# Kernel tuning notes

Hardware: AMD Instinct MI355X
Metric: run time of the kernel (lower is better)

The kernel has to match this reference:

```python
import jax, jax.numpy as jnp
import numpy as np

N_NODES = 50000


def _gcn_conv(h, src, dst, W, b):
    # h: [N, d_in] -> [N, d_out]; symmetric-normalized aggregation with self-loops
    N = h.shape[0]
    h = h @ W  # transform first (d_out < d_in), like PyG GCNConv
    deg = jax.ops.segment_sum(jnp.ones_like(dst, dtype=h.dtype), dst, num_segments=N)
    dinv = jnp.where(deg > 0, jax.lax.rsqrt(jnp.maximum(deg, 1.0)), 0.0)
    norm = dinv[src] * dinv[dst]  # [E']
    msg = h[src] * norm[:, None]  # [E', d_out]
    out = jax.ops.segment_sum(msg, dst, num_segments=N)
    return out + b


def setup_inputs() -> dict:
    key = jax.random.key(0)
    k1, k2, k3, k4 = jax.random.split(key, 4)
    dim_in, dim_h, dim_out, E = 512, 96, 40, 800000
    x = jax.random.normal(k1, (N_NODES, dim_in), dtype=jnp.float32)
    edge_index = jax.random.randint(k2, (2, E), 0, N_NODES, dtype=jnp.int64)
    W1 = jax.random.normal(k3, (dim_in, dim_h), dtype=jnp.float32) / np.sqrt(dim_in)
    b1 = jnp.zeros((dim_h,), dtype=jnp.float32)
    W2 = jax.random.normal(k4, (dim_h, dim_out), dtype=jnp.float32) / np.sqrt(dim_h)
    b2 = jnp.zeros((dim_out,), dtype=jnp.float32)
    return {"x": x, "edge_index": edge_index, "W1": W1, "b1": b1, "W2": W2, "b2": b2}


def reference(x, edge_index, W1, b1, W2, b2):
    N = x.shape[0]
    loops = jnp.arange(N, dtype=edge_index.dtype)
    src = jnp.concatenate([edge_index[0], loops])
    dst = jnp.concatenate([edge_index[1], loops])
    h = jax.nn.relu(_gcn_conv(x, src, dst, W1, b1))
    # dropout p=0.5 is identity in eval mode (training=False)
    logits = _gcn_conv(h, src, dst, W2, b2)
    return (logits, jax.nn.log_softmax(logits, axis=1))
```

## Files before the change

kernel.cpp:

```cpp
#include <hip/hip_runtime.h>
#include <cstdint>
#include <cstddef>

#define DIN 512
#define DH  96
#define DOUT 40

typedef __attribute__((ext_vector_type(8))) short s8v;
typedef __attribute__((ext_vector_type(4))) float f4v;

__device__ __forceinline__ ushort f2bf(float f) {
    uint u = __float_as_uint(f);
    u += 0x7fffu + ((u >> 16) & 1u);
    return (ushort)(u >> 16);
}
__device__ __forceinline__ float bflo(uint u) { return __uint_as_float(u << 16); }
__device__ __forceinline__ float bfhi(uint u) { return __uint_as_float(u & 0xffff0000u); }

__global__ __launch_bounds__(256) void k_prep(
    const float* __restrict__ W1, const float* __restrict__ W2,
    int* __restrict__ cnt, ushort* __restrict__ W1T, ushort* __restrict__ W2T, int N)
{
    int i = blockIdx.x * 256 + threadIdx.x;
    if (i < N) cnt[i] = 0;
    if (i < DIN * DH) {
        int k = i / DH, n = i % DH;
        W1T[(size_t)n * DIN + k] = f2bf(W1[i]);
    }
    if (i < 48 * DH) {
        int n = i / DH, k = i % DH;
        W2T[i] = (n < DOUT) ? f2bf(W2[(size_t)k * DOUT + n]) : (ushort)0;
    }
}

__global__ __launch_bounds__(256) void k_hist(const int* __restrict__ dst, int* __restrict__ cnt, int E) {
    int e = blockIdx.x * 256 + threadIdx.x;
    if (e < E) atomicAdd(&cnt[dst[e]], 1);
}

__global__ __launch_bounds__(256) void k_blocksum(const int* __restrict__ cnt, int* __restrict__ bsum, int N) {
    int i = blockIdx.x * 256 + threadIdx.x;
    int c = (i < N) ? cnt[i] : 0;
    #pragma unroll
    for (int off = 32; off >= 1; off >>= 1) c += __shfl_down(c, off, 64);
    __shared__ int wsum[4];
    if ((threadIdx.x & 63) == 0) wsum[threadIdx.x >> 6] = c;
    __syncthreads();
    if (threadIdx.x == 0) bsum[blockIdx.x] = wsum[0] + wsum[1] + wsum[2] + wsum[3];
}

__global__ __launch_bounds__(256) void k_scan_small(const int* __restrict__ bsum, int* __restrict__ boff, int SB) {
    __shared__ int p[256];
    int tid = threadIdx.x;
    int v = (tid < SB) ? bsum[tid] : 0;
    p[tid] = v;
    __syncthreads();
    #pragma unroll
    for (int off = 1; off < 256; off <<= 1) {
        int t = (tid >= off) ? p[tid - off] : 0;
        __syncthreads();
        p[tid] += t;
        __syncthreads();
    }
    if (tid < SB) boff[tid] = p[tid] - v;
}

__global__ __launch_bounds__(256) void k_rowptr(
    const int* __restrict__ cnt, const int* __restrict__ boff,
    int* __restrict__ row_ptr, int* __restrict__ cursor,
    float* __restrict__ dinv, int N)
{
    __shared__ int p[256];
    int tid = threadIdx.x;
    int i = blockIdx.x * 256 + tid;
    int c = (i < N) ? cnt[i] : 0;
    p[tid] = c;
    __syncthreads();
    #pragma unroll
    for (int off = 1; off < 256; off <<= 1) {
        int t = (tid >= off) ? p[tid - off] : 0;
        __syncthreads();
        p[tid] += t;
        __syncthreads();
    }
    int excl = p[tid] - c;
    if (i < N) {
        int base = boff[blockIdx.x] + excl;
        row_ptr[i] = base;
        cursor[i]  = base;
        dinv[i] = rsqrtf(1.0f + (float)c);
        if (i == N - 1) row_ptr[N] = base + c;
    }
}

__global__ __launch_bounds__(256) void k_fill(
    const int* __restrict__ src, const int* __restrict__ dst,
    int* __restrict__ cursor, int* __restrict__ adj, int E)
{
    int e = blockIdx.x * 256 + threadIdx.x;
    if (e >= E) return;
    int pos = atomicAdd(&cursor[dst[e]], 1);
    adj[pos] = src[e];
}

#define G1_ASZ 8192
#define G1_BSZ 6144
__global__ __launch_bounds__(256) void k_gemm1(
    const float* __restrict__ x, const ushort* __restrict__ W1T,
    const float* __restrict__ dinv, ushort* __restrict__ hs1, int N)
{
    __shared__ ushort lds[2 * G1_ASZ + 2 * G1_BSZ];
    const int tid = threadIdx.x;
    const int row0 = blockIdx.x * 128;
    const int lane = tid & 63;
    const int w = tid >> 6;
    const int rb = (w >> 1) * 64;
    const int cb = (w & 1) * 48;
    const int lm = lane & 15;
    const int lq = lane >> 4;

    int aof[4][2], bof[3][2];
    #pragma unroll
    for (int i = 0; i < 4; ++i)
        #pragma unroll
        for (int ks = 0; ks < 2; ++ks) {
            int r = rb + i * 16 + lm;
            int c = ks * 32 + lq * 8;
            aof[i][ks] = r * 64 + (c ^ ((r & 7) << 3));
        }
    #pragma unroll
    for (int j = 0; j < 3; ++j)
        #pragma unroll
        for (int ks = 0; ks < 2; ++ks) {
            int n = cb + j * 16 + lm;
            int c = ks * 32 + lq * 8;
            bof[j][ks] = 2 * G1_ASZ + n * 64 + (c ^ ((n & 7) << 3));
        }

    f4v acc[4][3];
    #pragma unroll
    for (int i = 0; i < 4; ++i)
        #pragma unroll
        for (int j = 0; j < 3; ++j) acc[i][j] = (f4v)0.f;

    const int sr = tid >> 1;
    const int scb = (tid & 1) * 32;

    auto stage = [&](int kt, int buf) {
        int k0 = kt * 64;
        int gr = row0 + sr;
        ushort* A = lds + buf * G1_ASZ;
        #pragma unroll
        for (int s = 0; s < 4; ++s) {
            int c = scb + s * 8;
            float4 v0 = make_float4(0.f, 0.f, 0.f, 0.f), v1 = v0;
            if (gr < N) {
                const float* p = &x[(size_t)gr * DIN + k0 + c];
                v0 = *(const float4*)p;
                v1 = *(const float4*)(p + 4);
            }
            uint4 wv;
            wv.x = (uint)f2bf(v0.x) | ((uint)f2bf(v0.y) << 16);
            wv.y = (uint)f2bf(v0.z) | ((uint)f2bf(v0.w) << 16);
            wv.z = (uint)f2bf(v1.x) | ((uint)f2bf(v1.y) << 16);
            wv.w = (uint)f2bf(v1.z) | ((uint)f2bf(v1.w) << 16);
            *(uint4*)&A[sr * 64 + (c ^ ((sr & 7) << 3))] = wv;
        }
        ushort* B = lds + 2 * G1_ASZ + buf * G1_BSZ;
        #pragma unroll
        for (int it = 0; it < 3; ++it) {
            int ss = tid + it * 256;
            int n = ss >> 3, c = (ss & 7) * 8;
            uint4 wv = *(const uint4*)&W1T[(size_t)n * DIN + k0 + c];
            *(uint4*)&B[n * 64 + (c ^ ((n & 7) << 3))] = wv;
        }
    };

    stage(0, 0);
    for (int kt = 0; kt < 8; ++kt) {
        __syncthreads();
        if (kt < 7) stage(kt + 1, (kt + 1) & 1);
        const int ab = (kt & 1) * G1_ASZ;
        const int bb = (kt & 1) * G1_BSZ;
        #pragma unroll
        for (int ks = 0; ks < 2; ++ks) {
            s8v b0 = *(s8v*)&lds[bof[0][ks] + bb];
            s8v b1 = *(s8v*)&lds[bof[1][ks] + bb];
            s8v b2 = *(s8v*)&lds[bof[2][ks] + bb];
            #pragma unroll
            for (int i = 0; i < 4; ++i) {
                s8v a = *(s8v*)&lds[aof[i][ks] + ab];
                acc[i][0] = __builtin_amdgcn_mfma_f32_16x16x32_bf16(a, b0, acc[i][0], 0, 0, 0);
                acc[i][1] = __builtin_amdgcn_mfma_f32_16x16x32_bf16(a, b1, acc[i][1], 0, 0, 0);
                acc[i][2] = __builtin_amdgcn_mfma_f32_16x16x32_bf16(a, b2, acc[i][2], 0, 0, 0);
            }
        }
    }

    #pragma unroll
    for (int i = 0; i < 4; ++i) {
        int gr0 = row0 + rb + i * 16 + lq * 4;
        #pragma unroll
        for (int q = 0; q < 4; ++q) {
            int gr = gr0 + q;
            if (gr < N) {
                float di = dinv[gr];
                #pragma unroll
                for (int j = 0; j < 3; ++j)
                    hs1[(size_t)gr * DH + cb + j * 16 + lm] = f2bf(acc[i][j][q] * di);
            }
        }
    }
}

__global__ __launch_bounds__(256) void k_agg1(
    const int* __restrict__ row_ptr, const int* __restrict__ adj,
    const float* __restrict__ dinv, const ushort* __restrict__ hs1,
    const float* __restrict__ b1, ushort* __restrict__ h1, int N)
{
    int t = blockIdx.x * 256 + threadIdx.x;
    int node = t >> 6, lane = t & 63;
    if (node >= N) return;
    int c = lane << 1;
    const bool act = (c < DH);

    float a0 = 0.f, a1 = 0.f;
    if (act) {
        uint u = *(const uint*)&hs1[(size_t)node * DH + c];
        a0 = bflo(u); a1 = bfhi(u);
    }
    int e = row_ptr[node], e1 = row_ptr[node + 1];
    for (; e + 3 < e1; e += 4) {
        int s0 = adj[e], s1 = adj[e + 1], s2 = adj[e + 2], s3 = adj[e + 3];
        if (act) {
            uint u0 = *(const uint*)&hs1[(size_t)s0 * DH + c];
            uint u1 = *(const uint*)&hs1[(size_t)s1 * DH + c];
            uint u2 = *(const uint*)&hs1[(size_t)s2 * DH + c];
            uint u3 = *(const uint*)&hs1[(size_t)s3 * DH + c];
            a0 += bflo(u0); a1 += bfhi(u0);
            a0 += bflo(u1); a1 += bfhi(u1);
            a0 += bflo(u2); a1 += bfhi(u2);
            a0 += bflo(u3); a1 += bfhi(u3);
        }
    }
    for (; e < e1; ++e) {
        int s = adj[e];
        if (act) {
            uint u = *(const uint*)&hs1[(size_t)s * DH + c];
            a0 += bflo(u); a1 += bfhi(u);
        }
    }
    if (act) {
        float di = dinv[node];
        float r0 = fmaxf(fmaf(a0, di, b1[c]), 0.f);
        float r1 = fmaxf(fmaf(a1, di, b1[c + 1]), 0.f);
        uint wv = (uint)f2bf(r0) | ((uint)f2bf(r1) << 16);
        *(uint*)&h1[(size_t)node * DH + c] = wv;
    }
}

#define G2_HS 16384
__global__ __launch_bounds__(256) void k_gemm2(
    const ushort* __restrict__ h1, const ushort* __restrict__ W2T,
    const float* __restrict__ dinv, float* __restrict__ hs2, int N)
{
    __shared__ ushort lds[G2_HS + 48 * 128];
    const int tid = threadIdx.x;
    const int row0 = blockIdx.x * 128;

    for (int f = tid; f < 576; f += 256) {
        int r = f / 12, c = (f % 12) * 8;
        uint4 v = *(const uint4*)&W2T[r * DH + c];
        *(uint4*)&lds[G2_HS + r * 128 + (c ^ ((r & 7) << 3))] = v;
    }
    {
        int r = tid >> 1, half = tid & 1;
        int gr = row0 + r;
        #pragma unroll
        for (int i = 0; i < 6; ++i) {
            int c = half * 48 + i * 8;
            uint4 v = make_uint4(0, 0, 0, 0);
            if (gr < N) v = *(const uint4*)&h1[(size_t)gr * DH + c];
            *(uint4*)&lds[r * 128 + (c ^ ((r & 7) << 3))] = v;
        }
    }
    __syncthreads();

    const int lane = tid & 63, w = tid >> 6;
    const int rb = w * 32, lm = lane & 15, lq = lane >> 4;
    f4v acc[2][3];
    #pragma unroll
    for (int i = 0; i < 2; ++i)
        #pragma unroll
        for (int j = 0; j < 3; ++j) acc[i][j] = (f4v)0.f;

    #pragma unroll
    for (int ks = 0; ks < 3; ++ks) {
        int kk = ks * 32 + lq * 8;
        s8v b[3];
        #pragma unroll
        for (int j = 0; j < 3; ++j) {
            int n = j * 16 + lm;
            b[j] = *(s8v*)&lds[G2_HS + n * 128 + (kk ^ ((n & 7) << 3))];
        }
        #pragma unroll
        for (int i = 0; i < 2; ++i) {
            int r = rb + i * 16 + lm;
            s8v a = *(s8v*)&lds[r * 128 + (kk ^ ((r & 7) << 3))];
            #pragma unroll
            for (int j = 0; j < 3; ++j)
                acc[i][j] = __builtin_amdgcn_mfma_f32_16x16x32_bf16(a, b[j], acc[i][j], 0, 0, 0);
        }
    }

    #pragma unroll
    for (int i = 0; i < 2; ++i) {
        int gr0 = row0 + rb + i * 16 + lq * 4;
        #pragma unroll
        for (int q = 0; q < 4; ++q) {
            int gr = gr0 + q;
            if (gr < N) {
                float di = dinv[gr];
                #pragma unroll
                for (int j = 0; j < 3; ++j) {
                    int col = j * 16 + lm;
                    if (col < DOUT)
                        hs2[(size_t)gr * DOUT + col] = acc[i][j][q] * di;
                }
            }
        }
    }
}

__global__ __launch_bounds__(256) void k_agg2sm(
    const int* __restrict__ row_ptr, const int* __restrict__ adj,
    const float* __restrict__ dinv, const float* __restrict__ hs2,
    const float* __restrict__ b2, float* __restrict__ out,
    float* __restrict__ lsm, int N)
{
    int t = blockIdx.x * 256 + threadIdx.x;
    int node = t >> 6, lane = t & 63;
    if (node >= N) return;
    const bool act = lane < DOUT;

    float acc = act ? hs2[(size_t)node * DOUT + lane] : 0.f;
    int e = row_ptr[node], e1 = row_ptr[node + 1];
    for (; e + 3 < e1; e += 4) {
        int s0 = adj[e], s1 = adj[e + 1], s2 = adj[e + 2], s3 = adj[e + 3];
        if (act) {
            float v0 = hs2[(size_t)s0 * DOUT + lane];
            float v1 = hs2[(size_t)s1 * DOUT + lane];
            float v2 = hs2[(size_t)s2 * DOUT + lane];
            float v3 = hs2[(size_t)s3 * DOUT + lane];
            acc += v0 + v1 + v2 + v3;
        }
    }
    for (; e < e1; ++e) {
        int s = adj[e];
        if (act) acc += hs2[(size_t)s * DOUT + lane];
    }

    float v = act ? fmaf(acc, dinv[node], b2[lane]) : -1e30f;
    float m = v;
    #pragma unroll
    for (int off = 32; off >= 1; off >>= 1) m = fmaxf(m, __shfl_xor(m, off));
    float ex = act ? __expf(v - m) : 0.f;
    float s = ex;
    #pragma unroll
    for (int off = 32; off >= 1; off >>= 1) s += __shfl_xor(s, off);
    float lse = m + __logf(s);
    if (act) {
        out[(size_t)node * DOUT + lane] = v;
        lsm[(size_t)node * DOUT + lane] = v - lse;
    }
}

extern "C" void kernel_launch(void* const* d_in, const int* in_sizes, int n_in,
                              void* d_out, int out_size, void* d_ws, size_t ws_size,
                              hipStream_t stream) {
    const float* x  = (const float*)d_in[0];
    const int*   ei = (const int*)d_in[1];
    const float* W1 = (const float*)d_in[2];
    const float* b1 = (const float*)d_in[3];
    const float* W2 = (const float*)d_in[4];
    const float* b2 = (const float*)d_in[5];

    const int N = in_sizes[0] / DIN;
    const int E = in_sizes[1] / 2;
    const int* srcp = ei;
    const int* dstp = ei + E;
    const int SB = (N + 255) / 256;

    ushort* hs1 = (ushort*)d_ws;
    ushort* h1  = hs1 + (size_t)N * DH;
    float* hs2  = (float*)(h1 + (size_t)N * DH);
    float* dinv = hs2 + (size_t)N * DOUT;
    ushort* W1T = (ushort*)(dinv + N);
    ushort* W2T = W1T + (size_t)DH * DIN;
    int* cnt     = (int*)(W2T + 48 * DH);
    int* cursor  = cnt + N;
    int* row_ptr = cursor + N;
    int* adj     = row_ptr + N + 1;
    int* bsum    = adj + E;
    int* boff    = bsum + SB;

    float* out = (float*)d_out;
    float* lsm = out + (size_t)N * DOUT;

    const int gE = (E + 255) / 256;

    k_prep<<<SB, 256, 0, stream>>>(W1, W2, cnt, W1T, W2T, N);
    k_hist<<<gE, 256, 0, stream>>>(dstp, cnt, E);
    k_blocksum<<<SB, 256, 0, stream>>>(cnt, bsum, N);
    k_scan_small<<<1, 256, 0, stream>>>(bsum, boff, SB);
    k_rowptr<<<SB, 256, 0, stream>>>(cnt, boff, row_ptr, cursor, dinv, N);
    k_fill<<<gE, 256, 0, stream>>>(srcp, dstp, cursor, adj, E);

    k_gemm1<<<(N + 127) / 128, 256, 0, stream>>>(x, W1T, dinv, hs1, N);
    k_agg1<<<(int)(((size_t)N * 64 + 255) / 256), 256, 0, stream>>>(row_ptr, adj, dinv, hs1, b1, h1, N);

    k_gemm2<<<(N + 127) / 128, 256, 0, stream>>>(h1, W2T, dinv, hs2, N);
    k_agg2sm<<<(int)(((size_t)N * 64 + 255) / 256), 256, 0, stream>>>(row_ptr, adj, dinv, hs2, b2, out, lsm, N);
}
```

Before: 225.3 us.

## Fuse all GCN stages into one cooperative persistent kernel with grid syncs

Replaces the ten-kernel launch sequence with a single cooperative kernel of 512 blocks that runs CSR build, both GEMMs, both aggregations and log-softmax separated by grid-wide barriers. It falls back to the original multi-kernel path if the cooperative launch fails. The aim is to remove per-launch overhead and inter-kernel gaps. In exchange, the gather phases run with a fixed number of persistent waves, and grid barriers add their own synchronisation cost.

```diff
diff --git a/kernel.cpp b/kernel.cpp
--- a/kernel.cpp
+++ b/kernel.cpp
@@ -1,10 +1,17 @@
 #include <hip/hip_runtime.h>
+#include <hip/hip_cooperative_groups.h>
 #include <cstdint>
 #include <cstddef>
+
+namespace cg = cooperative_groups;
 
 #define DIN 512
 #define DH  96
 #define DOUT 40
+#define NBLK 512
+#define TPB  256
+#define NTHR (NBLK * TPB)
+#define NWAVE (NTHR / 64)
 
 typedef __attribute__((ext_vector_type(8))) short s8v;
 typedef __attribute__((ext_vector_type(4))) float f4v;
@@ -16,6 +23,343 @@
 }
 __device__ __forceinline__ float bflo(uint u) { return __uint_as_float(u << 16); }
 __device__ __forceinline__ float bfhi(uint u) { return __uint_as_float(u & 0xffff0000u); }
+
+struct Params {
+    const float* x; const int* src; const int* dst;
+    const float* W1; const float* b1; const float* W2; const float* b2;
+    ushort* hs1; ushort* h1; float* hs2; float* dinv;
+    ushort* W1T; ushort* W2T;
+    int* cnt; int* cursor; int* row_ptr; int* adj; int* bsum; int* boff;
+    float* out; float* lsm;
+    int N; int E;
+};
+
+__global__ void __launch_bounds__(TPB, 2) k_mega(Params p) {
+    cg::grid_group grid = cg::this_grid();
+    __shared__ __align__(16) ushort lds[28672];
+    int* ldsI = (int*)lds;
+
+    const int bid = blockIdx.x, tid = threadIdx.x;
+    const int gtid = bid * TPB + tid;
+    const int N = p.N, E = p.E;
+
+    for (int i = gtid; i < N; i += NTHR) p.cnt[i] = 0;
+    for (int i = gtid; i < DIN * DH; i += NTHR) {
+        int k = i / DH, n = i % DH;
+        p.W1T[(size_t)n * DIN + k] = f2bf(p.W1[i]);
+    }
+    for (int i = gtid; i < 48 * DH; i += NTHR) {
+        int n = i / DH, k = i % DH;
+        p.W2T[i] = (n < DOUT) ? f2bf(p.W2[(size_t)k * DOUT + n]) : (ushort)0;
+    }
+    grid.sync();
+
+    for (int e = gtid; e < E; e += NTHR) atomicAdd(&p.cnt[p.dst[e]], 1);
+    grid.sync();
+
+    {
+        int i = gtid;
+        int c = (i < N) ? p.cnt[i] : 0;
+        int s = c;
+        #pragma unroll
+        for (int off = 32; off >= 1; off >>= 1) s += __shfl_down(s, off, 64);
+        if ((tid & 63) == 0) ldsI[tid >> 6] = s;
+        __syncthreads();
+        if (tid == 0) p.bsum[bid] = ldsI[0] + ldsI[1] + ldsI[2] + ldsI[3];
+    }
+    grid.sync();
+
+    if (bid == 0) {
+        __syncthreads();
+        int v0 = p.bsum[tid], v1 = p.bsum[tid + 256];
+        ldsI[tid] = v0; ldsI[tid + 256] = v1;
+        __syncthreads();
+        for (int off = 1; off < 512; off <<= 1) {
+            int a0 = (tid >= off) ? ldsI[tid - off] : 0;
+            int a1 = (tid + 256 >= off) ? ldsI[tid + 256 - off] : 0;
+            __syncthreads();
+            ldsI[tid] += a0; ldsI[tid + 256] += a1;
+            __syncthreads();
+        }
+        p.boff[tid] = ldsI[tid] - v0;
+        p.boff[tid + 256] = ldsI[tid + 256] - v1;
+    }
+    grid.sync();
+
+    {
+        int i = gtid;
+        int c = (i < N) ? p.cnt[i] : 0;
+        ldsI[tid] = c;
+        __syncthreads();
+        for (int off = 1; off < 256; off <<= 1) {
+            int a = (tid >= off) ? ldsI[tid - off] : 0;
+            __syncthreads();
+            ldsI[tid] += a;
+            __syncthreads();
+        }
+        int excl = ldsI[tid] - c;
+        if (i < N) {
+            int base = p.boff[bid] + excl;
+            p.row_ptr[i] = base;
+            p.cursor[i]  = base;
+            p.dinv[i] = rsqrtf(1.0f + (float)c);
+            if (i == N - 1) p.row_ptr[N] = base + c;
+        }
+    }
+    grid.sync();
+
+    for (int e = gtid; e < E; e += NTHR) {
+        int pos = atomicAdd(&p.cursor[p.dst[e]], 1);
+        p.adj[pos] = p.src[e];
+    }
+    grid.sync();
+
+    {
+        const int lane = tid & 63, w = tid >> 6;
+        const int rb = (w >> 1) * 64, cb = (w & 1) * 48;
+        const int lm = lane & 15, lq = lane >> 4;
+        int aof[4][2], bof[3][2];
+        #pragma unroll
+        for (int i = 0; i < 4; ++i)
+            #pragma unroll
+            for (int ks = 0; ks < 2; ++ks) {
+                int r = rb + i * 16 + lm, c = ks * 32 + lq * 8;
+                aof[i][ks] = r * 64 + (c ^ ((r & 7) << 3));
+            }
+        #pragma unroll
+        for (int j = 0; j < 3; ++j)
+            #pragma unroll
+            for (int ks = 0; ks < 2; ++ks) {
+                int n = cb + j * 16 + lm, c = ks * 32 + lq * 8;
+                bof[j][ks] = 16384 + n * 64 + (c ^ ((n & 7) << 3));
+            }
+        const int sr = tid >> 1, scb = (tid & 1) * 32;
+        const int ntile = (N + 127) / 128;
+
+        for (int t = bid; t < ntile; t += NBLK) {
+            const int row0 = t * 128;
+            f4v acc[4][3];
+            #pragma unroll
+            for (int i = 0; i < 4; ++i)
+                #pragma unroll
+                for (int j = 0; j < 3; ++j) acc[i][j] = (f4v)0.f;
+
+            auto stage = [&](int kt, int buf) {
+                int k0 = kt * 64;
+                int gr = row0 + sr;
+                ushort* A = lds + buf * 8192;
+                #pragma unroll
+                for (int s = 0; s < 4; ++s) {
+                    int c = scb + s * 8;
+                    float4 v0 = make_float4(0.f, 0.f, 0.f, 0.f), v1 = v0;
+                    if (gr < N) {
+                        const float* pp = &p.x[(size_t)gr * DIN + k0 + c];
+                        v0 = *(const float4*)pp;
+                        v1 = *(const float4*)(pp + 4);
+                    }
+                    uint4 wv;
+                    wv.x = (uint)f2bf(v0.x) | ((uint)f2bf(v0.y) << 16);
+                    wv.y = (uint)f2bf(v0.z) | ((uint)f2bf(v0.w) << 16);
+                    wv.z = (uint)f2bf(v1.x) | ((uint)f2bf(v1.y) << 16);
+                    wv.w = (uint)f2bf(v1.z) | ((uint)f2bf(v1.w) << 16);
+                    *(uint4*)&A[sr * 64 + (c ^ ((sr & 7) << 3))] = wv;
+                }
+                ushort* B = lds + 16384 + buf * 6144;
+                #pragma unroll
+                for (int it = 0; it < 3; ++it) {
+                    int ss = tid + it * 256;
+                    int n = ss >> 3, c = (ss & 7) * 8;
+                    uint4 wv = *(const uint4*)&p.W1T[(size_t)n * DIN + k0 + c];
+                    *(uint4*)&B[n * 64 + (c ^ ((n & 7) << 3))] = wv;
+                }
+            };
+
+            __syncthreads();
+            stage(0, 0);
+            for (int kt = 0; kt < 8; ++kt) {
+                __syncthreads();
+                if (kt < 7) stage(kt + 1, (kt + 1) & 1);
+                const int ab = (kt & 1) * 8192;
+                const int bb = (kt & 1) * 6144;
+                #pragma unroll
+                for (int ks = 0; ks < 2; ++ks) {
+                    s8v b0 = *(s8v*)&lds[bof[0][ks] + bb];
+                    s8v b1 = *(s8v*)&lds[bof[1][ks] + bb];
+                    s8v b2 = *(s8v*)&lds[bof[2][ks] + bb];
+                    #pragma unroll
+                    for (int i = 0; i < 4; ++i) {
+                        s8v a = *(s8v*)&lds[aof[i][ks] + ab];
+                        acc[i][0] = __builtin_amdgcn_mfma_f32_16x16x32_bf16(a, b0, acc[i][0], 0, 0, 0);
+                        acc[i][1] = __builtin_amdgcn_mfma_f32_16x16x32_bf16(a, b1, acc[i][1], 0, 0, 0);
+                        acc[i][2] = __builtin_amdgcn_mfma_f32_16x16x32_bf16(a, b2, acc[i][2], 0, 0, 0);
+                    }
+                }
+            }
+            #pragma unroll
+            for (int i = 0; i < 4; ++i) {
+                int gr0 = row0 + rb + i * 16 + lq * 4;
+                #pragma unroll
+                for (int q = 0; q < 4; ++q) {
+                    int gr = gr0 + q;
+                    if (gr < N) {
+                        float di = p.dinv[gr];
+                        #pragma unroll
+                        for (int j = 0; j < 3; ++j)
+                            p.hs1[(size_t)gr * DH + cb + j * 16 + lm] = f2bf(acc[i][j][q] * di);
+                    }
+                }
+            }
+        }
+    }
+    grid.sync();
+
+    {
+        const int lane = tid & 63;
+        const int wid = gtid >> 6;
+        const int c = lane << 1;
+        const bool act = (c < DH);
+        for (int node = wid; node < N; node += NWAVE) {
+            float a0 = 0.f, a1 = 0.f;
+            if (act) {
+                uint u = *(const uint*)&p.hs1[(size_t)node * DH + c];
+                a0 = bflo(u); a1 = bfhi(u);
+            }
+            int e = p.row_ptr[node], e1 = p.row_ptr[node + 1];
+            for (; e + 3 < e1; e += 4) {
+                int s0 = p.adj[e], s1 = p.adj[e + 1], s2 = p.adj[e + 2], s3 = p.adj[e + 3];
+                if (act) {
+                    uint u0 = *(const uint*)&p.hs1[(size_t)s0 * DH + c];
+                    uint u1 = *(const uint*)&p.hs1[(size_t)s1 * DH + c];
+                    uint u2 = *(const uint*)&p.hs1[(size_t)s2 * DH + c];
+                    uint u3 = *(const uint*)&p.hs1[(size_t)s3 * DH + c];
+                    a0 += bflo(u0); a1 += bfhi(u0);
+                    a0 += bflo(u1); a1 += bfhi(u1);
+                    a0 += bflo(u2); a1 += bfhi(u2);
+                    a0 += bflo(u3); a1 += bfhi(u3);
+                }
+            }
+            for (; e < e1; ++e) {
+                int s = p.adj[e];
+                if (act) {
+                    uint u = *(const uint*)&p.hs1[(size_t)s * DH + c];
+                    a0 += bflo(u); a1 += bfhi(u);
+                }
+            }
+            if (act) {
+                float di = p.dinv[node];
+                float r0 = fmaxf(fmaf(a0, di, p.b1[c]), 0.f);
+                float r1 = fmaxf(fmaf(a1, di, p.b1[c + 1]), 0.f);
+                *(uint*)&p.h1[(size_t)node * DH + c] = (uint)f2bf(r0) | ((uint)f2bf(r1) << 16);
+            }
+        }
+    }
+    grid.sync();
+
+    {
+        for (int f = tid; f < 576; f += 256) {
+            int r = f / 12, c = (f % 12) * 8;
+            uint4 v = *(const uint4*)&p.W2T[r * DH + c];
+            *(uint4*)&lds[16384 + r * 128 + (c ^ ((r & 7) << 3))] = v;
+        }
+        const int lane = tid & 63, w = tid >> 6;
+        const int rb = w * 32, lm = lane & 15, lq = lane >> 4;
+        const int ntile = (N + 127) / 128;
+
+        for (int t = bid; t < ntile; t += NBLK) {
+            const int row0 = t * 128;
+            __syncthreads();
+            {
+                int r = tid >> 1, half = tid & 1;
+                int gr = row0 + r;
+                #pragma unroll
+                for (int i = 0; i < 6; ++i) {
+                    int c = half * 48 + i * 8;
+                    uint4 v = make_uint4(0, 0, 0, 0);
+                    if (gr < N) v = *(const uint4*)&p.h1[(size_t)gr * DH + c];
+                    *(uint4*)&lds[r * 128 + (c ^ ((r & 7) << 3))] = v;
+                }
+            }
+            __syncthreads();
+
+            f4v acc[2][3];
+            #pragma unroll
+            for (int i = 0; i < 2; ++i)
+                #pragma unroll
+                for (int j = 0; j < 3; ++j) acc[i][j] = (f4v)0.f;
+
+            #pragma unroll
+            for (int ks = 0; ks < 3; ++ks) {
+                int kk = ks * 32 + lq * 8;
+                s8v b[3];
+                #pragma unroll
+                for (int j = 0; j < 3; ++j) {
+                    int n = j * 16 + lm;
+                    b[j] = *(s8v*)&lds[16384 + n * 128 + (kk ^ ((n & 7) << 3))];
+                }
+                #pragma unroll
+                for (int i = 0; i < 2; ++i) {
+                    int r = rb + i * 16 + lm;
+                    s8v a = *(s8v*)&lds[r * 128 + (kk ^ ((r & 7) << 3))];
+                    #pragma unroll
+                    for (int j = 0; j < 3; ++j)
+                        acc[i][j] = __builtin_amdgcn_mfma_f32_16x16x32_bf16(a, b[j], acc[i][j], 0, 0, 0);
+                }
+            }
+            #pragma unroll
+            for (int i = 0; i < 2; ++i) {
+                int gr0 = row0 + rb + i * 16 + lq * 4;
+                #pragma unroll
+                for (int q = 0; q < 4; ++q) {
+                    int gr = gr0 + q;
+                    if (gr < N) {
+                        float di = p.dinv[gr];
+                        #pragma unroll
+                        for (int j = 0; j < 3; ++j) {
+                            int col = j * 16 + lm;
+                            if (col < DOUT)
+                                p.hs2[(size_t)gr * DOUT + col] = acc[i][j][q] * di;
+                        }
+                    }
+                }
+            }
+        }
+    }
+    grid.sync();
+
+    {
+        const int lane = tid & 63;
+        const int wid = gtid >> 6;
+        const bool act = lane < DOUT;
+        for (int node = wid; node < N; node += NWAVE) {
+            float acc = act ? p.hs2[(size_t)node * DOUT + lane] : 0.f;
+            int e = p.row_ptr[node], e1 = p.row_ptr[node + 1];
+            for (; e + 3 < e1; e += 4) {
+                int s0 = p.adj[e], s1 = p.adj[e + 1], s2 = p.adj[e + 2], s3 = p.adj[e + 3];
+                if (act) {
+                    acc += p.hs2[(size_t)s0 * DOUT + lane] + p.hs2[(size_t)s1 * DOUT + lane]
+                         + p.hs2[(size_t)s2 * DOUT + lane] + p.hs2[(size_t)s3 * DOUT + lane];
+                }
+            }
+            for (; e < e1; ++e) {
+                int s = p.adj[e];
+                if (act) acc += p.hs2[(size_t)s * DOUT + lane];
+            }
+            float v = act ? fmaf(acc, p.dinv[node], p.b2[lane]) : -1e30f;
+            float m = v;
+            #pragma unroll
+            for (int off = 32; off >= 1; off >>= 1) m = fmaxf(m, __shfl_xor(m, off));
+            float ex = act ? __expf(v - m) : 0.f;
+            float s = ex;
+            #pragma unroll
+            for (int off = 32; off >= 1; off >>= 1) s += __shfl_xor(s, off);
+            float lse = m + __logf(s);
+            if (act) {
+                p.out[(size_t)node * DOUT + lane] = v;
+                p.lsm[(size_t)node * DOUT + lane] = v - lse;
+            }
+        }
+    }
+}
 
 __global__ __launch_bounds__(256) void k_prep(
     const float* __restrict__ W1, const float* __restrict__ W2,
@@ -50,19 +394,19 @@
 }
 
 __global__ __launch_bounds__(256) void k_scan_small(const int* __restrict__ bsum, int* __restrict__ boff, int SB) {
-    __shared__ int p[256];
+    __shared__ int pp[256];
     int tid = threadIdx.x;
     int v = (tid < SB) ? bsum[tid] : 0;
-    p[tid] = v;
+    pp[tid] = v;
     __syncthreads();
     #pragma unroll
     for (int off = 1; off < 256; off <<= 1) {
-        int t = (tid >= off) ? p[tid - off] : 0;
-        __syncthreads();
-        p[tid] += t;
-        __syncthreads();
-    }
-    if (tid < SB) boff[tid] = p[tid] - v;
+        int t = (tid >= off) ? pp[tid - off] : 0;
+        __syncthreads();
+        pp[tid] += t;
+        __syncthreads();
+    }
+    if (tid < SB) boff[tid] = pp[tid] - v;
 }
 
 __global__ __launch_bounds__(256) void k_rowptr(
@@ -70,20 +414,20 @@
     int* __restrict__ row_ptr, int* __restrict__ cursor,
     float* __restrict__ dinv, int N)
 {
-    __shared__ int p[256];
+    __shared__ int pp[256];
     int tid = threadIdx.x;
     int i = blockIdx.x * 256 + tid;
     int c = (i < N) ? cnt[i] : 0;
-    p[tid] = c;
+    pp[tid] = c;
     __syncthreads();
     #pragma unroll
     for (int off = 1; off < 256; off <<= 1) {
-        int t = (tid >= off) ? p[tid - off] : 0;
-        __syncthreads();
-        p[tid] += t;
-        __syncthreads();
-    }
-    int excl = p[tid] - c;
+        int t = (tid >= off) ? pp[tid - off] : 0;
+        __syncthreads();
+        pp[tid] += t;
+        __syncthreads();
+    }
+    int excl = pp[tid] - c;
     if (i < N) {
         int base = boff[blockIdx.x] + excl;
         row_ptr[i] = base;
@@ -103,38 +447,31 @@
     adj[pos] = src[e];
 }
 
-#define G1_ASZ 8192
-#define G1_BSZ 6144
-__global__ __launch_bounds__(256) void k_gemm1(
+__global__ __launch_bounds__(256) void k_gemm1s(
     const float* __restrict__ x, const ushort* __restrict__ W1T,
     const float* __restrict__ dinv, ushort* __restrict__ hs1, int N)
 {
-    __shared__ ushort lds[2 * G1_ASZ + 2 * G1_BSZ];
+    __shared__ __align__(16) ushort lds[28672];
     const int tid = threadIdx.x;
     const int row0 = blockIdx.x * 128;
-    const int lane = tid & 63;
-    const int w = tid >> 6;
-    const int rb = (w >> 1) * 64;
-    const int cb = (w & 1) * 48;
-    const int lm = lane & 15;
-    const int lq = lane >> 4;
+    const int lane = tid & 63, w = tid >> 6;
+    const int rb = (w >> 1) * 64, cb = (w & 1) * 48;
+    const int lm = lane & 15, lq = lane >> 4;
 
     int aof[4][2], bof[3][2];
     #pragma unroll
     for (int i = 0; i < 4; ++i)
         #pragma unroll
         for (int ks = 0; ks < 2; ++ks) {
-            int r = rb + i * 16 + lm;
-            int c = ks * 32 + lq * 8;
+            int r = rb + i * 16 + lm, c = ks * 32 + lq * 8;
             aof[i][ks] = r * 64 + (c ^ ((r & 7) << 3));
         }
     #pragma unroll
     for (int j = 0; j < 3; ++j)
         #pragma unroll
         for (int ks = 0; ks < 2; ++ks) {
-            int n = cb + j * 16 + lm;
-            int c = ks * 32 + lq * 8;
-            bof[j][ks] = 2 * G1_ASZ + n * 64 + (c ^ ((n & 7) << 3));
+            int n = cb + j * 16 + lm, c = ks * 32 + lq * 8;
+            bof[j][ks] = 16384 + n * 64 + (c ^ ((n & 7) << 3));
         }
 
     f4v acc[4][3];
@@ -143,21 +480,20 @@
         #pragma unroll
         for (int j = 0; j < 3; ++j) acc[i][j] = (f4v)0.f;
 
-    const int sr = tid >> 1;
-    const int scb = (tid & 1) * 32;
+    const int sr = tid >> 1, scb = (tid & 1) * 32;
 
     auto stage = [&](int kt, int buf) {
         int k0 = kt * 64;
         int gr = row0 + sr;
-        ushort* A = lds + buf * G1_ASZ;
+        ushort* A = lds + buf * 8192;
         #pragma unroll
         for (int s = 0; s < 4; ++s) {
             int c = scb + s * 8;
             float4 v0 = make_float4(0.f, 0.f, 0.f, 0.f), v1 = v0;
             if (gr < N) {
-                const float* p = &x[(size_t)gr * DIN + k0 + c];
-                v0 = *(const float4*)p;
-                v1 = *(const float4*)(p + 4);
+                const float* pp = &x[(size_t)gr * DIN + k0 + c];
+                v0 = *(const float4*)pp;
+                v1 = *(const float4*)(pp + 4);
             }
             uint4 wv;
             wv.x = (uint)f2bf(v0.x) | ((uint)f2bf(v0.y) << 16);
@@ -166,7 +502,7 @@
             wv.w = (uint)f2bf(v1.z) | ((uint)f2bf(v1.w) << 16);
             *(uint4*)&A[sr * 64 + (c ^ ((sr & 7) << 3))] = wv;
         }
-        ushort* B = lds + 2 * G1_ASZ + buf * G1_BSZ;
+        ushort* B = lds + 16384 + buf * 6144;
         #pragma unroll
         for (int it = 0; it < 3; ++it) {
             int ss = tid + it * 256;
@@ -180,8 +516,8 @@
     for (int kt = 0; kt < 8; ++kt) {
         __syncthreads();
         if (kt < 7) stage(kt + 1, (kt + 1) & 1);
-        const int ab = (kt & 1) * G1_ASZ;
-        const int bb = (kt & 1) * G1_BSZ;
+        const int ab = (kt & 1) * 8192;
+        const int bb = (kt & 1) * 6144;
         #pragma unroll
         for (int ks = 0; ks < 2; ++ks) {
             s8v b0 = *(s8v*)&lds[bof[0][ks] + bb];
@@ -254,24 +590,22 @@
         float di = dinv[node];
         float r0 = fmaxf(fmaf(a0, di, b1[c]), 0.f);
         float r1 = fmaxf(fmaf(a1, di, b1[c + 1]), 0.f);
-        uint wv = (uint)f2bf(r0) | ((uint)f2bf(r1) << 16);
-        *(uint*)&h1[(size_t)node * DH + c] = wv;
-    }
-}
-
-#define G2_HS 16384
-__global__ __launch_bounds__(256) void k_gemm2(
+        *(uint*)&h1[(size_t)node * DH + c] = (uint)f2bf(r0) | ((uint)f2bf(r1) << 16);
+    }
+}
+
+__global__ __launch_bounds__(256) void k_gemm2s(
     const ushort* __restrict__ h1, const ushort* __restrict__ W2T,
     const float* __restrict__ dinv, float* __restrict__ hs2, int N)
 {
-    __shared__ ushort lds[G2_HS + 48 * 128];
+    __shared__ __align__(16) ushort lds[16384 + 48 * 128];
     const int tid = threadIdx.x;
     const int row0 = blockIdx.x * 128;
 
     for (int f = tid; f < 576; f += 256) {
         int r = f / 12, c = (f % 12) * 8;
         uint4 v = *(const uint4*)&W2T[r * DH + c];
-        *(uint4*)&lds[G2_HS + r * 128 + (c ^ ((r & 7) << 3))] = v;
+        *(uint4*)&lds[16384 + r * 128 + (c ^ ((r & 7) << 3))] = v;
     }
     {
         int r = tid >> 1, half = tid & 1;
@@ -301,7 +635,7 @@
         #pragma unroll
         for (int j = 0; j < 3; ++j) {
             int n = j * 16 + lm;
-            b[j] = *(s8v*)&lds[G2_HS + n * 128 + (kk ^ ((n & 7) << 3))];
+            b[j] = *(s8v*)&lds[16384 + n * 128 + (kk ^ ((n & 7) << 3))];
         }
         #pragma unroll
         for (int i = 0; i < 2; ++i) {
@@ -348,11 +682,8 @@
     for (; e + 3 < e1; e += 4) {
         int s0 = adj[e], s1 = adj[e + 1], s2 = adj[e + 2], s3 = adj[e + 3];
         if (act) {
-            float v0 = hs2[(size_t)s0 * DOUT + lane];
-            float v1 = hs2[(size_t)s1 * DOUT + lane];
-            float v2 = hs2[(size_t)s2 * DOUT + lane];
-            float v3 = hs2[(size_t)s3 * DOUT + lane];
-            acc += v0 + v1 + v2 + v3;
+            acc += hs2[(size_t)s0 * DOUT + lane] + hs2[(size_t)s1 * DOUT + lane]
+                 + hs2[(size_t)s2 * DOUT + lane] + hs2[(size_t)s3 * DOUT + lane];
         }
     }
     for (; e < e1; ++e) {
@@ -389,7 +720,6 @@
     const int E = in_sizes[1] / 2;
     const int* srcp = ei;
     const int* dstp = ei + E;
-    const int SB = (N + 255) / 256;
 
     ushort* hs1 = (ushort*)d_ws;
     ushort* h1  = hs1 + (size_t)N * DH;
@@ -402,23 +732,36 @@
     int* row_ptr = cursor + N;
     int* adj     = row_ptr + N + 1;
     int* bsum    = adj + E;
-    int* boff    = bsum + SB;
+    int* boff    = bsum + NBLK;
 
     float* out = (float*)d_out;
     float* lsm = out + (size_t)N * DOUT;
 
+    Params prm;
+    prm.x = x; prm.src = srcp; prm.dst = dstp;
+    prm.W1 = W1; prm.b1 = b1; prm.W2 = W2; prm.b2 = b2;
+    prm.hs1 = hs1; prm.h1 = h1; prm.hs2 = hs2; prm.dinv = dinv;
+    prm.W1T = W1T; prm.W2T = W2T;
+    prm.cnt = cnt; prm.cursor = cursor; prm.row_ptr = row_ptr; prm.adj = adj;
+    prm.bsum = bsum; prm.boff = boff;
+    prm.out = out; prm.lsm = lsm;
+    prm.N = N; prm.E = E;
+
+    void* args[] = { &prm };
+    hipError_t err = hipLaunchCooperativeKernel((const void*)k_mega, dim3(NBLK), dim3(TPB),
+                                                args, 0, stream);
+    if (err == hipSuccess) return;
+
+    const int SB = (N + 255) / 256;
     const int gE = (E + 255) / 256;
-
     k_prep<<<SB, 256, 0, stream>>>(W1, W2, cnt, W1T, W2T, N);
     k_hist<<<gE, 256, 0, stream>>>(dstp, cnt, E);
     k_blocksum<<<SB, 256, 0, stream>>>(cnt, bsum, N);
     k_scan_small<<<1, 256, 0, stream>>>(bsum, boff, SB);
     k_rowptr<<<SB, 256, 0, stream>>>(cnt, boff, row_ptr, cursor, dinv, N);
     k_fill<<<gE, 256, 0, stream>>>(srcp, dstp, cursor, adj, E);
-
-    k_gemm1<<<(N + 127) / 128, 256, 0, stream>>>(x, W1T, dinv, hs1, N);
+    k_gemm1s<<<(N + 127) / 128, 256, 0, stream>>>(x, W1T, dinv, hs1, N);
     k_agg1<<<(int)(((size_t)N * 64 + 255) / 256), 256, 0, stream>>>(row_ptr, adj, dinv, hs1, b1, h1, N);
-
-    k_gemm2<<<(N + 127) / 128, 256, 0, stream>>>(h1, W2T, dinv, hs2, N);
+    k_gemm2s<<<(N + 127) / 128, 256, 0, stream>>>(h1, W2T, dinv, hs2, N);
     k_agg2sm<<<(int)(((size_t)N * 64 + 255) / 256), 256, 0, stream>>>(row_ptr, adj, dinv, hs2, b2, out, lsm, N);
 }
```

Result: slower. 878.4 us (+289.8%).
